# Kernel optimization log

Measured on AMD Instinct MI355X. Metric: run time of the kernel, lower is better.

Reference implementation:

```python
import jax, jax.numpy as jnp
import numpy as np

NEG = -1e30

def setup_inputs() -> dict:
    key = jax.random.key(0)
    k1, k2, k3, k4, k5 = jax.random.split(key, 5)
    B, N, M, D = 32, 2048, 512, 512
    C = jax.random.normal(k1, (B, N, D), dtype=jnp.float32)
    Q = jax.random.normal(k2, (B, M, D), dtype=jnp.float32)
    Cmask = jax.random.randint(k3, (B, N), 0, 2, dtype=jnp.int32)
    Qmask = jax.random.randint(k4, (B, M), 0, 2, dtype=jnp.int32)
    # Linear(3*dim, 1, bias=False) weight, flattened to a (3*dim,) vector.
    bound = 1.0 / np.sqrt(3 * D)
    w = jax.random.uniform(k5, (3 * D,), dtype=jnp.float32, minval=-bound, maxval=bound)
    return {"C": C, "Q": Q, "Cmask": Cmask, "Qmask": Qmask, "w": w}

def reference(C, Q, Cmask, Qmask, w):
    D = C.shape[-1]
    w1, w2, w3 = w[:D], w[D:2 * D], w[2 * D:]
    # Trilinear similarity, decomposed: S = w1.Ct + w2.Qt + w3.(Ct*Qt)
    S = (jnp.einsum('bnd,d->bn', C, w1)[:, :, None]
         + jnp.einsum('bmd,d->bm', Q, w2)[:, None, :]
         + jnp.einsum('bnd,bmd->bnm', C * w3, Q))  # [B, N, M]
    Qm = Qmask.astype(S.dtype)[:, None, :]  # [B, 1, M]; 1 = masked
    Cm = Cmask.astype(S.dtype)[:, :, None]  # [B, N, 1]
    S1 = jax.nn.softmax(S * (1.0 - Qm) + Qm * NEG, axis=2)
    S2 = jax.nn.softmax(S * (1.0 - Cm) + Cm * NEG, axis=1)
    A = jnp.einsum('bnm,bmd->bnd', S1, Q)
    T = jnp.einsum('bnm,bnd->bmd', S2, C)     # S2^T @ C
    Bout = jnp.einsum('bnm,bmd->bnd', S1, T)  # S1 @ (S2^T @ C)
    return (A, Bout)
```

## Files before the change

### kernel.cpp

```cpp
#include <hip/hip_runtime.h>

#define BB 32
#define NN 2048
#define MM 512
#define DD 512

typedef _Float16 half8f __attribute__((ext_vector_type(8)));
typedef float    f32x16 __attribute__((ext_vector_type(16)));

#define MFMA __builtin_amdgcn_mfma_f32_32x32x16_f16

__device__ __forceinline__ int pidx(int r, int k, int K) {
    return (r >> 7) * (K << 7) + ((k >> 4) << 11) + (((r >> 5) & 3) << 9)
         + (((r & 31) + (((k >> 3) & 1) << 5)) << 3) + (k & 7);
}
__device__ __forceinline__ int kpart(int k) {
    return ((k >> 4) << 11) + (((k >> 3) & 1) << 8) + (k & 7);
}

__device__ __forceinline__ void glds16(const void* g, void* l) {
    __builtin_amdgcn_global_load_lds(
        (const __attribute__((address_space(1))) unsigned int*)g,
        (__attribute__((address_space(3))) unsigned int*)l, 16, 0, 0);
}

__global__ __launch_bounds__(256) void k_prepC(const float* __restrict__ C, const float* __restrict__ w,
                                               float* __restrict__ c1, _Float16* __restrict__ PCt,
                                               _Float16* __restrict__ PCh, _Float16* __restrict__ PCl) {
    __shared__ float Ls[64][65];
    const int bid = blockIdx.x;
    const int b   = bid >> 8;
    const int nn0 = ((bid >> 3) & 31) << 6;
    const int dd0 = (bid & 7) << 6;
    const int tid = threadIdx.x;
    const int nl  = tid >> 2;
    const int dl  = (tid & 3) << 4;
    const float* w1 = w;
    const float* w3 = w + 2 * DD;
    const size_t crow = ((size_t)(b * NN + nn0 + nl)) * DD + dd0 + dl;
    float4 v[4], u[4], t[4];
#pragma unroll
    for (int p = 0; p < 4; ++p) {
        v[p] = *(const float4*)(C + crow + p * 4);
        u[p] = *(const float4*)(w1 + dd0 + dl + p * 4);
        t[p] = *(const float4*)(w3 + dd0 + dl + p * 4);
    }
    float s = 0.f;
#pragma unroll
    for (int p = 0; p < 4; ++p) s += v[p].x * u[p].x + v[p].y * u[p].y + v[p].z * u[p].z + v[p].w * u[p].w;
    s += __shfl_xor(s, 1); s += __shfl_xor(s, 2);
    if ((tid & 3) == 0) atomicAdd(&c1[b * NN + nn0 + nl], s);
#pragma unroll
    for (int p = 0; p < 4; ++p) {
        Ls[dl + p * 4 + 0][nl] = v[p].x; Ls[dl + p * 4 + 1][nl] = v[p].y;
        Ls[dl + p * 4 + 2][nl] = v[p].z; Ls[dl + p * 4 + 3][nl] = v[p].w;
    }
    const size_t pb = (size_t)b * NN * DD;
#pragma unroll
    for (int q = 0; q < 2; ++q) {
        float x[8];
#pragma unroll
        for (int e = 0; e < 8; ++e) {
            const int p = q * 2 + (e >> 2);
            const float* vp = &v[p].x; const float* tp = &t[p].x;
            x[e] = vp[e & 3] * tp[e & 3];
        }
        half8f hh, ll;
#pragma unroll
        for (int e = 0; e < 8; ++e) {
            _Float16 h = (_Float16)x[e]; hh[e] = h;
            ll[e] = (_Float16)((x[e] - (float)h) * 2048.f);
        }
        const int pi = pidx(nn0 + nl, dd0 + dl + q * 8, DD);
        *(half8f*)&PCh[pb + pi] = hh;
        *(half8f*)&PCl[pb + pi] = ll;
    }
    __syncthreads();
    const int d2 = tid >> 2, n2 = (tid & 3) << 4;
    const size_t tb = (size_t)b * DD * NN;
#pragma unroll
    for (int q = 0; q < 2; ++q) {
        const int nc = n2 + q * 8;
        half8f o;
#pragma unroll
        for (int j = 0; j < 8; ++j) o[j] = (_Float16)Ls[d2][nc + j];
        *(half8f*)&PCt[tb + pidx(dd0 + d2, nn0 + nc, NN)] = o;
    }
}

__global__ __launch_bounds__(256) void k_prepQ(const float* __restrict__ Q, const int* __restrict__ Qmask,
                                               const float* __restrict__ w, float* __restrict__ q2,
                                               _Float16* __restrict__ PQt,
                                               _Float16* __restrict__ PQh, _Float16* __restrict__ PQl) {
    __shared__ float Ls[64][65];
    const int bid = blockIdx.x;
    const int b   = bid >> 6;
    const int rem = bid & 63;
    const int mm0 = (rem >> 3) << 6;
    const int dd0 = (rem & 7) << 6;
    const int tid = threadIdx.x;
    const int ml  = tid >> 2;
    const int dl  = (tid & 3) << 4;
    const float* w2 = w + DD;
    const size_t qrow = ((size_t)(b * MM + mm0 + ml)) * DD + dd0 + dl;
    float4 v[4], u[4];
#pragma unroll
    for (int p = 0; p < 4; ++p) {
        v[p] = *(const float4*)(Q + qrow + p * 4);
        u[p] = *(const float4*)(w2 + dd0 + dl + p * 4);
    }
    float s = 0.f;
#pragma unroll
    for (int p = 0; p < 4; ++p) s += v[p].x * u[p].x + v[p].y * u[p].y + v[p].z * u[p].z + v[p].w * u[p].w;
    s += __shfl_xor(s, 1); s += __shfl_xor(s, 2);
    if ((tid & 3) == 0) atomicAdd(&q2[b * MM + mm0 + ml], s);
    const float z = Qmask[b * MM + mm0 + ml] ? 0.f : 1.f;
#pragma unroll
    for (int p = 0; p < 4; ++p) {
        Ls[dl + p * 4 + 0][ml] = v[p].x * z; Ls[dl + p * 4 + 1][ml] = v[p].y * z;
        Ls[dl + p * 4 + 2][ml] = v[p].z * z; Ls[dl + p * 4 + 3][ml] = v[p].w * z;
    }
    const size_t pb = (size_t)b * MM * DD;
#pragma unroll
    for (int q = 0; q < 2; ++q) {
        float x[8];
#pragma unroll
        for (int e = 0; e < 8; ++e) {
            const int p = q * 2 + (e >> 2);
            const float* vp = &v[p].x;
            x[e] = vp[e & 3];
        }
        half8f hh, ll;
#pragma unroll
        for (int e = 0; e < 8; ++e) {
            _Float16 h = (_Float16)x[e]; hh[e] = h;
            ll[e] = (_Float16)((x[e] - (float)h) * 2048.f);
        }
        const int pi = pidx(mm0 + ml, dd0 + dl + q * 8, DD);
        *(half8f*)&PQh[pb + pi] = hh;
        *(half8f*)&PQl[pb + pi] = ll;
    }
    __syncthreads();
    const int d2 = tid >> 2, m2 = (tid & 3) << 4;
    const size_t tb = (size_t)b * DD * MM;
#pragma unroll
    for (int q = 0; q < 2; ++q) {
        const int mc = m2 + q * 8;
        half8f o;
#pragma unroll
        for (int j = 0; j < 8; ++j) o[j] = (_Float16)Ls[d2][mc + j];
        *(half8f*)&PQt[tb + pidx(dd0 + d2, mm0 + mc, MM)] = o;
    }
}

__global__ __launch_bounds__(256) void k_te(const _Float16* __restrict__ PE, const int* __restrict__ Cmask,
                                            _Float16* __restrict__ PEt) {
    __shared__ float Ls[64][65];
    const int bid = blockIdx.x;
    const int b   = bid >> 8;
    const int nn0 = ((bid >> 3) & 31) << 6;
    const int mm0 = (bid & 7) << 6;
    const int tid = threadIdx.x;
    const int nl  = tid >> 2;
    const int ml  = (tid & 3) << 4;
    const float z = Cmask[b * NN + nn0 + nl] ? 0.f : 1.f;
    const size_t eb = (size_t)b * NN * MM;
#pragma unroll
    for (int q = 0; q < 2; ++q) {
        half8f v = *(const half8f*)&PE[eb + pidx(nn0 + nl, mm0 + ml + q * 8, MM)];
#pragma unroll
        for (int j = 0; j < 8; ++j) Ls[ml + q * 8 + j][nl] = (float)v[j] * z;
    }
    __syncthreads();
    const int m2 = tid >> 2, n2 = (tid & 3) << 4;
    const size_t tb = (size_t)b * MM * NN;
#pragma unroll
    for (int q = 0; q < 2; ++q) {
        const int nc = n2 + q * 8;
        half8f o;
#pragma unroll
        for (int j = 0; j < 8; ++j) o[j] = (_Float16)Ls[m2][nc + j];
        *(half8f*)&PEt[tb + pidx(mm0 + m2, nn0 + nc, NN)] = o;
    }
}

__global__ __launch_bounds__(256, 2) void k_sgemm(const _Float16* __restrict__ PCh, const _Float16* __restrict__ PCl,
                                                  const _Float16* __restrict__ PQh, const _Float16* __restrict__ PQl,
                                                  const int* __restrict__ Cmask, const int* __restrict__ Qmask,
                                                  const float* __restrict__ c1, const float* __restrict__ q2,
                                                  _Float16* __restrict__ E, float* __restrict__ rsum,
                                                  float* __restrict__ csum) {
    __shared__ _Float16 SB[2][16384];
    __shared__ float rowp[128], colp[128], cmz[128], qmz[128], c1s[128], q2s[128];
    const int hw  = blockIdx.x;
    const int bid = ((hw & 7) << 8) | (hw >> 3);
    const int b   = bid >> 6;
    const int rem = bid & 63;
    const int n0  = (rem >> 2) << 7;
    const int m0  = (rem & 3) << 7;
    const int tid = threadIdx.x;
    const int lane = tid & 63;
    const int wv   = tid >> 6;
    const int wr = wv >> 1, wc = wv & 1;
    if (tid < 128) {
        rowp[tid] = 0.f; colp[tid] = 0.f;
        cmz[tid] = Cmask[b * NN + n0 + tid] ? 0.f : 1.f;
        c1s[tid] = c1[b * NN + n0 + tid];
    } else {
        const int t = tid - 128;
        qmz[t] = Qmask[b * MM + m0 + t] ? 0.f : 1.f;
        q2s[t] = q2[b * MM + m0 + t];
    }
    const half8f* gAh = (const half8f*)(PCh + (size_t)b * NN * DD + (size_t)n0 * DD) + lane;
    const half8f* gAl = (const half8f*)(PCl + (size_t)b * NN * DD + (size_t)n0 * DD) + lane;
    const half8f* gBh = (const half8f*)(PQh + (size_t)b * MM * DD + (size_t)m0 * DD) + lane;
    const half8f* gBl = (const half8f*)(PQl + (size_t)b * MM * DD + (size_t)m0 * DD) + lane;
    const half8f* srcj[8]; int offj[8];
#pragma unroll
    for (int j = 0; j < 8; ++j) {
        const int f = j * 4 + wv;
        const int kcl = f >> 4, t = f & 15;
        const half8f* s; int p;
        if (t < 4)       { s = gAh; p = t; }
        else if (t < 8)  { s = gAl; p = t - 4; }
        else if (t < 12) { s = gBh; p = t - 8; }
        else             { s = gBl; p = t - 12; }
        srcj[j] = s + kcl * 256 + p * 64;
        offj[j] = (kcl * 16 + t) << 9;
    }
    f32x16 accH[2][2] = {};
    f32x16 accX[2][2] = {};
#pragma unroll
    for (int j = 0; j < 8; ++j) glds16(srcj[j], &SB[0][offj[j]]);
    int cur = 0;
    for (int ks = 0; ks < 16; ++ks) {
        __syncthreads();
        if (ks + 1 < 16) {
#pragma unroll
            for (int j = 0; j < 8; ++j) glds16(srcj[j] + (ks + 1) * 512, &SB[cur ^ 1][offj[j]]);
        }
#pragma unroll
        for (int kcl = 0; kcl < 2; ++kcl) {
            const _Float16* F = &SB[cur][(kcl << 13) + lane * 8];
            half8f ah0 = *(const half8f*)(F + ((2 * wr) << 9));
            half8f ah1 = *(const half8f*)(F + ((2 * wr + 1) << 9));
            half8f al0 = *(const half8f*)(F + ((4 + 2 * wr) << 9));
            half8f al1 = *(const half8f*)(F + ((5 + 2 * wr) << 9));
            half8f bh0 = *(const half8f*)(F + ((8 + 2 * wc) << 9));
            half8f bh1 = *(const half8f*)(F + ((9 + 2 * wc) << 9));
            half8f bl0 = *(const half8f*)(F + ((12 + 2 * wc) << 9));
            half8f bl1 = *(const half8f*)(F + ((13 + 2 * wc) << 9));
            accH[0][0] = MFMA(ah0, bh0, accH[0][0], 0, 0, 0);
            accH[0][1] = MFMA(ah0, bh1, accH[0][1], 0, 0, 0);
            accH[1][0] = MFMA(ah1, bh0, accH[1][0], 0, 0, 0);
            accH[1][1] = MFMA(ah1, bh1, accH[1][1], 0, 0, 0);
            accX[0][0] = MFMA(ah0, bl0, accX[0][0], 0, 0, 0);
            accX[0][0] = MFMA(al0, bh0, accX[0][0], 0, 0, 0);
            accX[0][1] = MFMA(ah0, bl1, accX[0][1], 0, 0, 0);
            accX[0][1] = MFMA(al0, bh1, accX[0][1], 0, 0, 0);
            accX[1][0] = MFMA(ah1, bl0, accX[1][0], 0, 0, 0);
            accX[1][0] = MFMA(al1, bh0, accX[1][0], 0, 0, 0);
            accX[1][1] = MFMA(ah1, bl1, accX[1][1], 0, 0, 0);
            accX[1][1] = MFMA(al1, bh1, accX[1][1], 0, 0, 0);
        }
        cur ^= 1;
    }
    const float inv2k = 4.8828125e-4f;
    const int mcol0 = wc * 64 + (lane & 31);
    const float qz0 = qmz[mcol0], qz1 = qmz[mcol0 + 32];
    const float q2v0 = q2s[mcol0], q2v1 = q2s[mcol0 + 32];
    const int hi4 = (lane >> 5) << 2;
    const size_t ebase = (size_t)b * NN * MM + (size_t)n0 * MM;
    const int kp0 = kpart(m0 + mcol0);
    const int kp1 = kpart(m0 + mcol0 + 32);
    float colacc0 = 0.f, colacc1 = 0.f;
#pragma unroll
    for (int i = 0; i < 2; ++i) {
#pragma unroll
        for (int r = 0; r < 16; ++r) {
            const int nloc = wr * 64 + i * 32 + (r & 3) + ((r >> 2) << 3) + hi4;
            const float base = c1s[nloc];
            float S0 = accH[i][0][r] + accX[i][0][r] * inv2k + base + q2v0;
            float S1 = accH[i][1][r] + accX[i][1][r] * inv2k + base + q2v1;
            float e0 = __expf(S0), e1 = __expf(S1);
            _Float16 h0 = (_Float16)e0, h1 = (_Float16)e1;
            float eq0 = (float)h0, eq1 = (float)h1;
            const int rp = (((nloc >> 5) & 3) << 9) + ((nloc & 31) << 3);
            E[ebase + rp + kp0] = h0;
            E[ebase + rp + kp1] = h1;
            const float cz = cmz[nloc];
            colacc0 += eq0 * cz;
            colacc1 += eq1 * cz;
            float rv = eq0 * qz0 + eq1 * qz1;
            rv += __shfl_xor(rv, 1);  rv += __shfl_xor(rv, 2);
            rv += __shfl_xor(rv, 4);  rv += __shfl_xor(rv, 8);
            rv += __shfl_xor(rv, 16);
            if ((lane & 31) == 0) atomicAdd(&rowp[nloc], rv);
        }
    }
    atomicAdd(&colp[mcol0], colacc0);
    atomicAdd(&colp[mcol0 + 32], colacc1);
    __syncthreads();
    if (tid < 128) atomicAdd(&rsum[b * NN + n0 + tid], rowp[tid]);
    else atomicAdd(&csum[b * MM + m0 + tid - 128], colp[tid - 128]);
}

__global__ __launch_bounds__(256, 2) void k_T(const _Float16* __restrict__ PCt,
                                              const _Float16* __restrict__ PEt,
                                              const float* __restrict__ csum,
                                              const int* __restrict__ Qmask,
                                              _Float16* __restrict__ Tt) {
    __shared__ _Float16 SB[2][16384];
    const int hw  = blockIdx.x;
    const int bid = ((hw & 7) << 6) | (hw >> 3);
    const int b   = bid >> 4;
    const int rem = bid & 15;
    const int d0  = (rem >> 2) << 7;
    const int m0  = (rem & 3) << 7;
    const int tid = threadIdx.x;
    const int lane = tid & 63;
    const int wv   = tid >> 6;
    const int wr = wv >> 1, wc = wv & 1;
    const half8f* gA = (const half8f*)(PCt + (size_t)b * DD * NN + (size_t)d0 * NN) + lane;
    const half8f* gB = (const half8f*)(PEt + (size_t)b * MM * NN + (size_t)m0 * NN) + lane;
    const half8f* srcj[8]; int offj[8];
#pragma unroll
    for (int j = 0; j < 8; ++j) {
        const int f = j * 4 + wv;
        const int kcl = f >> 3, t = f & 7;
        const half8f* s; int p;
        if (t < 4) { s = gA; p = t; } else { s = gB; p = t - 4; }
        srcj[j] = s + kcl * 256 + p * 64;
        offj[j] = (kcl * 8 + t) << 9;
    }
    f32x16 acc[2][2] = {};
#pragma unroll
    for (int j = 0; j < 8; ++j) glds16(srcj[j], &SB[0][offj[j]]);
    int cur = 0;
    for (int ks = 0; ks < 32; ++ks) {
        __syncthreads();
        if (ks + 1 < 32) {
#pragma unroll
            for (int j = 0; j < 8; ++j) glds16(srcj[j] + (ks + 1) * 1024, &SB[cur ^ 1][offj[j]]);
        }
#pragma unroll
        for (int kcl = 0; kcl < 4; ++kcl) {
            const _Float16* F = &SB[cur][(kcl << 12) + lane * 8];
            half8f a0 = *(const half8f*)(F + ((2 * wr) << 9));
            half8f a1 = *(const half8f*)(F + ((2 * wr + 1) << 9));
            half8f b0 = *(const half8f*)(F + ((4 + 2 * wc) << 9));
            half8f b1 = *(const half8f*)(F + ((5 + 2 * wc) << 9));
            acc[0][0] = MFMA(a0, b0, acc[0][0], 0, 0, 0);
            acc[0][1] = MFMA(a0, b1, acc[0][1], 0, 0, 0);
            acc[1][0] = MFMA(a1, b0, acc[1][0], 0, 0, 0);
            acc[1][1] = MFMA(a1, b1, acc[1][1], 0, 0, 0);
        }
        cur ^= 1;
    }
    const int mc0 = m0 + wc * 64 + (lane & 31);
    const float s0 = (Qmask[b * MM + mc0]      ? 0.f : 1.f) / csum[b * MM + mc0];
    const float s1 = (Qmask[b * MM + mc0 + 32] ? 0.f : 1.f) / csum[b * MM + mc0 + 32];
    const int hi4 = (lane >> 5) << 2;
    const size_t tbase = (size_t)b * DD * MM + (size_t)d0 * MM;
    const int kp0 = kpart(mc0);
    const int kp1 = kpart(mc0 + 32);
#pragma unroll
    for (int i = 0; i < 2; ++i) {
#pragma unroll
        for (int r = 0; r < 16; ++r) {
            const int dloc = wr * 64 + i * 32 + (r & 3) + ((r >> 2) << 3) + hi4;
            const int rp = (((dloc >> 5) & 3) << 9) + ((dloc & 31) << 3);
            Tt[tbase + rp + kp0] = (_Float16)(acc[i][0][r] * s0);
            Tt[tbase + rp + kp1] = (_Float16)(acc[i][1][r] * s1);
        }
    }
}

__global__ __launch_bounds__(256, 2) void k_AB(const _Float16* __restrict__ E,
                                               const _Float16* __restrict__ PQt,
                                               const _Float16* __restrict__ Tt,
                                               const float* __restrict__ rsum,
                                               float* __restrict__ outA, float* __restrict__ outB) {
    __shared__ _Float16 SB[2][12288];
    const int hw  = blockIdx.x;
    const int bid = ((hw & 7) << 8) | (hw >> 3);
    const int b   = bid >> 6;
    const int rem = bid & 63;
    const int n0  = (rem >> 2) << 7;
    const int d0  = (rem & 3) << 7;
    const int tid = threadIdx.x;
    const int lane = tid & 63;
    const int wv   = tid >> 6;
    const int wr = wv >> 1, wc = wv & 1;
    const half8f* gE = (const half8f*)(E   + (size_t)b * NN * MM + (size_t)n0 * MM) + lane;
    const half8f* gQ = (const half8f*)(PQt + (size_t)b * DD * MM + (size_t)d0 * MM) + lane;
    const half8f* gT = (const half8f*)(Tt  + (size_t)b * DD * MM + (size_t)d0 * MM) + lane;
    const half8f* srcj[6]; int offj[6];
#pragma unroll
    for (int j = 0; j < 6; ++j) {
        const int f = j * 4 + wv;
        const int kcl = (f >= 12) ? 1 : 0;
        const int t = f - kcl * 12;
        const half8f* s; int p;
        if (t < 4)      { s = gE; p = t; }
        else if (t < 8) { s = gQ; p = t - 4; }
        else            { s = gT; p = t - 8; }
        srcj[j] = s + kcl * 256 + p * 64;
        offj[j] = (kcl * 12 + t) << 9;
    }
    f32x16 accA[2][2] = {};
    f32x16 accB[2][2] = {};
#pragma unroll
    for (int j = 0; j < 6; ++j) glds16(srcj[j], &SB[0][offj[j]]);
    int cur = 0;
    for (int ks = 0; ks < 16; ++ks) {
        __syncthreads();
        if (ks + 1 < 16) {
#pragma unroll
            for (int j = 0; j < 6; ++j) glds16(srcj[j] + (ks + 1) * 512, &SB[cur ^ 1][offj[j]]);
        }
#pragma unroll
        for (int kcl = 0; kcl < 2; ++kcl) {
            const _Float16* F = &SB[cur][kcl * 6144 + lane * 8];
            half8f e0 = *(const half8f*)(F + ((2 * wr) << 9));
            half8f e1 = *(const half8f*)(F + ((2 * wr + 1) << 9));
            half8f q0 = *(const half8f*)(F + ((4 + 2 * wc) << 9));
            half8f q1 = *(const half8f*)(F + ((5 + 2 * wc) << 9));
            half8f t0 = *(const half8f*)(F + ((8 + 2 * wc) << 9));
            half8f t1 = *(const half8f*)(F + ((9 + 2 * wc) << 9));
            accA[0][0] = MFMA(e0, q0, accA[0][0], 0, 0, 0);
            accA[0][1] = MFMA(e0, q1, accA[0][1], 0, 0, 0);
            accA[1][0] = MFMA(e1, q0, accA[1][0], 0, 0, 0);
            accA[1][1] = MFMA(e1, q1, accA[1][1], 0, 0, 0);
            accB[0][0] = MFMA(e0, t0, accB[0][0], 0, 0, 0);
            accB[0][1] = MFMA(e0, t1, accB[0][1], 0, 0, 0);
            accB[1][0] = MFMA(e1, t0, accB[1][0], 0, 0, 0);
            accB[1][1] = MFMA(e1, t1, accB[1][1], 0, 0, 0);
        }
        cur ^= 1;
    }
    const int dc = d0 + wc * 64 + (lane & 31);
#pragma unroll
    for (int i = 0; i < 2; ++i) {
#pragma unroll
        for (int r = 0; r < 16; ++r) {
            const int row = (r & 3) + ((r >> 2) << 3) + ((lane >> 5) << 2);
            const int n = n0 + wr * 64 + i * 32 + row;
            const float inv = __builtin_amdgcn_rcpf(rsum[b * NN + n]);
            const size_t o = ((size_t)(b * NN + n)) * DD + dc;
            outA[o]      = accA[i][0][r] * inv;
            outA[o + 32] = accA[i][1][r] * inv;
            outB[o]      = accB[i][0][r] * inv;
            outB[o + 32] = accB[i][1][r] * inv;
        }
    }
}

extern "C" void kernel_launch(void* const* d_in, const int* in_sizes, int n_in,
                              void* d_out, int out_size, void* d_ws, size_t ws_size,
                              hipStream_t stream) {
    const float* C = (const float*)d_in[0];
    const float* Q = (const float*)d_in[1];
    const int* Cmask = (const int*)d_in[2];
    const int* Qmask = (const int*)d_in[3];
    const float* w  = (const float*)d_in[4];

    const size_t BNM = (size_t)BB * NN * MM;
    const size_t BMD = (size_t)BB * MM * DD;
    const size_t BND = (size_t)BB * NN * DD;
    const size_t BN  = (size_t)BB * NN;
    const size_t BM  = (size_t)BB * MM;

    _Float16* E   = (_Float16*)d_ws;
    _Float16* Tt  = E + BNM;
    _Float16* PQt = Tt + BMD;
    float* c1   = (float*)(PQt + BMD);
    float* q2   = c1 + BN;
    float* rsum = q2 + BM;
    float* csum = rsum + BN;

    _Float16* PCt = (_Float16*)d_out;
    _Float16* PCh = PCt + BND;
    _Float16* PCl = PCh + BND;
    _Float16* PQh = PCl + BND;
    _Float16* PQl = PQh + BMD;
    _Float16* PEt = PCh;

    hipMemsetAsync(c1, 0, 2 * (BN + BM) * sizeof(float), stream);

    k_prepQ<<<BB * 64, 256, 0, stream>>>(Q, Qmask, w, q2, PQt, PQh, PQl);
    k_prepC<<<BB * 256, 256, 0, stream>>>(C, w, c1, PCt, PCh, PCl);
    k_sgemm<<<2048, 256, 0, stream>>>(PCh, PCl, PQh, PQl, Cmask, Qmask, c1, q2, E, rsum, csum);
    k_te<<<BB * 256, 256, 0, stream>>>(E, Cmask, PEt);
    k_T<<<512, 256, 0, stream>>>(PCt, PEt, csum, Qmask, Tt);
    k_AB<<<2048, 256, 0, stream>>>(E, PQt, Tt, rsum,
                                   (float*)d_out, (float*)d_out + BND);
}
```

Before: 727.5 us.

## Drop hi/lo fp16 split in S GEMM and fuse E transpose into epilogue

The similarity GEMM no longer uses a split-fp16 (high plus scaled low residual) representation, so it computes one fp16 MFMA product instead of three and stops writing and reading the low-part buffers. The separate transpose kernel for E is removed; the GEMM epilogue now writes the Cmask-scaled transposed E directly with scattered scalar stores. The smaller LDS footprint allows launch bounds of three blocks per SM. The risk is lower accuracy in the logits before exp, plus uncoalesced 2-byte stores in the epilogue.

```diff
diff --git a/kernel.cpp b/kernel.cpp
--- a/kernel.cpp
+++ b/kernel.cpp
@@ -26,7 +26,7 @@
 
 __global__ __launch_bounds__(256) void k_prepC(const float* __restrict__ C, const float* __restrict__ w,
                                                float* __restrict__ c1, _Float16* __restrict__ PCt,
-                                               _Float16* __restrict__ PCh, _Float16* __restrict__ PCl) {
+                                               _Float16* __restrict__ PCh) {
     __shared__ float Ls[64][65];
     const int bid = blockIdx.x;
     const int b   = bid >> 8;
@@ -58,22 +58,14 @@
     const size_t pb = (size_t)b * NN * DD;
 #pragma unroll
     for (int q = 0; q < 2; ++q) {
-        float x[8];
+        half8f hh;
 #pragma unroll
         for (int e = 0; e < 8; ++e) {
             const int p = q * 2 + (e >> 2);
             const float* vp = &v[p].x; const float* tp = &t[p].x;
-            x[e] = vp[e & 3] * tp[e & 3];
-        }
-        half8f hh, ll;
-#pragma unroll
-        for (int e = 0; e < 8; ++e) {
-            _Float16 h = (_Float16)x[e]; hh[e] = h;
-            ll[e] = (_Float16)((x[e] - (float)h) * 2048.f);
-        }
-        const int pi = pidx(nn0 + nl, dd0 + dl + q * 8, DD);
-        *(half8f*)&PCh[pb + pi] = hh;
-        *(half8f*)&PCl[pb + pi] = ll;
+            hh[e] = (_Float16)(vp[e & 3] * tp[e & 3]);
+        }
+        *(half8f*)&PCh[pb + pidx(nn0 + nl, dd0 + dl + q * 8, DD)] = hh;
     }
     __syncthreads();
     const int d2 = tid >> 2, n2 = (tid & 3) << 4;
@@ -90,8 +82,7 @@
 
 __global__ __launch_bounds__(256) void k_prepQ(const float* __restrict__ Q, const int* __restrict__ Qmask,
                                                const float* __restrict__ w, float* __restrict__ q2,
-                                               _Float16* __restrict__ PQt,
-                                               _Float16* __restrict__ PQh, _Float16* __restrict__ PQl) {
+                                               _Float16* __restrict__ PQt, _Float16* __restrict__ PQh) {
     __shared__ float Ls[64][65];
     const int bid = blockIdx.x;
     const int b   = bid >> 6;
@@ -123,22 +114,14 @@
     const size_t pb = (size_t)b * MM * DD;
 #pragma unroll
     for (int q = 0; q < 2; ++q) {
-        float x[8];
+        half8f hh;
 #pragma unroll
         for (int e = 0; e < 8; ++e) {
             const int p = q * 2 + (e >> 2);
             const float* vp = &v[p].x;
-            x[e] = vp[e & 3];
-        }
-        half8f hh, ll;
-#pragma unroll
-        for (int e = 0; e < 8; ++e) {
-            _Float16 h = (_Float16)x[e]; hh[e] = h;
-            ll[e] = (_Float16)((x[e] - (float)h) * 2048.f);
-        }
-        const int pi = pidx(mm0 + ml, dd0 + dl + q * 8, DD);
-        *(half8f*)&PQh[pb + pi] = hh;
-        *(half8f*)&PQl[pb + pi] = ll;
+            hh[e] = (_Float16)vp[e & 3];
+        }
+        *(half8f*)&PQh[pb + pidx(mm0 + ml, dd0 + dl + q * 8, DD)] = hh;
     }
     __syncthreads();
     const int d2 = tid >> 2, m2 = (tid & 3) << 4;
@@ -153,44 +136,13 @@
     }
 }
 
-__global__ __launch_bounds__(256) void k_te(const _Float16* __restrict__ PE, const int* __restrict__ Cmask,
-                                            _Float16* __restrict__ PEt) {
-    __shared__ float Ls[64][65];
-    const int bid = blockIdx.x;
-    const int b   = bid >> 8;
-    const int nn0 = ((bid >> 3) & 31) << 6;
-    const int mm0 = (bid & 7) << 6;
-    const int tid = threadIdx.x;
-    const int nl  = tid >> 2;
-    const int ml  = (tid & 3) << 4;
-    const float z = Cmask[b * NN + nn0 + nl] ? 0.f : 1.f;
-    const size_t eb = (size_t)b * NN * MM;
-#pragma unroll
-    for (int q = 0; q < 2; ++q) {
-        half8f v = *(const half8f*)&PE[eb + pidx(nn0 + nl, mm0 + ml + q * 8, MM)];
-#pragma unroll
-        for (int j = 0; j < 8; ++j) Ls[ml + q * 8 + j][nl] = (float)v[j] * z;
-    }
-    __syncthreads();
-    const int m2 = tid >> 2, n2 = (tid & 3) << 4;
-    const size_t tb = (size_t)b * MM * NN;
-#pragma unroll
-    for (int q = 0; q < 2; ++q) {
-        const int nc = n2 + q * 8;
-        half8f o;
-#pragma unroll
-        for (int j = 0; j < 8; ++j) o[j] = (_Float16)Ls[m2][nc + j];
-        *(half8f*)&PEt[tb + pidx(mm0 + m2, nn0 + nc, NN)] = o;
-    }
-}
-
-__global__ __launch_bounds__(256, 2) void k_sgemm(const _Float16* __restrict__ PCh, const _Float16* __restrict__ PCl,
-                                                  const _Float16* __restrict__ PQh, const _Float16* __restrict__ PQl,
+__global__ __launch_bounds__(256, 3) void k_sgemm(const _Float16* __restrict__ PCh,
+                                                  const _Float16* __restrict__ PQh,
                                                   const int* __restrict__ Cmask, const int* __restrict__ Qmask,
                                                   const float* __restrict__ c1, const float* __restrict__ q2,
-                                                  _Float16* __restrict__ E, float* __restrict__ rsum,
-                                                  float* __restrict__ csum) {
-    __shared__ _Float16 SB[2][16384];
+                                                  _Float16* __restrict__ E, _Float16* __restrict__ PEt,
+                                                  float* __restrict__ rsum, float* __restrict__ csum) {
+    __shared__ _Float16 SB[2][8192];
     __shared__ float rowp[128], colp[128], cmz[128], qmz[128], c1s[128], q2s[128];
     const int hw  = blockIdx.x;
     const int bid = ((hw & 7) << 8) | (hw >> 3);
@@ -211,61 +163,40 @@
         qmz[t] = Qmask[b * MM + m0 + t] ? 0.f : 1.f;
         q2s[t] = q2[b * MM + m0 + t];
     }
-    const half8f* gAh = (const half8f*)(PCh + (size_t)b * NN * DD + (size_t)n0 * DD) + lane;
-    const half8f* gAl = (const half8f*)(PCl + (size_t)b * NN * DD + (size_t)n0 * DD) + lane;
-    const half8f* gBh = (const half8f*)(PQh + (size_t)b * MM * DD + (size_t)m0 * DD) + lane;
-    const half8f* gBl = (const half8f*)(PQl + (size_t)b * MM * DD + (size_t)m0 * DD) + lane;
-    const half8f* srcj[8]; int offj[8];
-#pragma unroll
-    for (int j = 0; j < 8; ++j) {
+    const half8f* gA = (const half8f*)(PCh + (size_t)b * NN * DD + (size_t)n0 * DD) + lane;
+    const half8f* gB = (const half8f*)(PQh + (size_t)b * MM * DD + (size_t)m0 * DD) + lane;
+    const half8f* srcj[4]; int offj[4];
+#pragma unroll
+    for (int j = 0; j < 4; ++j) {
         const int f = j * 4 + wv;
-        const int kcl = f >> 4, t = f & 15;
-        const half8f* s; int p;
-        if (t < 4)       { s = gAh; p = t; }
-        else if (t < 8)  { s = gAl; p = t - 4; }
-        else if (t < 12) { s = gBh; p = t - 8; }
-        else             { s = gBl; p = t - 12; }
-        srcj[j] = s + kcl * 256 + p * 64;
-        offj[j] = (kcl * 16 + t) << 9;
-    }
-    f32x16 accH[2][2] = {};
-    f32x16 accX[2][2] = {};
-#pragma unroll
-    for (int j = 0; j < 8; ++j) glds16(srcj[j], &SB[0][offj[j]]);
+        const int kcl = f >> 3, t = f & 7;
+        srcj[j] = (t < 4 ? gA + t * 64 : gB + (t - 4) * 64) + kcl * 256;
+        offj[j] = (kcl * 8 + t) << 9;
+    }
+    f32x16 acc[2][2] = {};
+#pragma unroll
+    for (int j = 0; j < 4; ++j) glds16(srcj[j], &SB[0][offj[j]]);
     int cur = 0;
     for (int ks = 0; ks < 16; ++ks) {
         __syncthreads();
         if (ks + 1 < 16) {
 #pragma unroll
-            for (int j = 0; j < 8; ++j) glds16(srcj[j] + (ks + 1) * 512, &SB[cur ^ 1][offj[j]]);
+            for (int j = 0; j < 4; ++j) glds16(srcj[j] + (ks + 1) * 512, &SB[cur ^ 1][offj[j]]);
         }
 #pragma unroll
         for (int kcl = 0; kcl < 2; ++kcl) {
-            const _Float16* F = &SB[cur][(kcl << 13) + lane * 8];
-            half8f ah0 = *(const half8f*)(F + ((2 * wr) << 9));
-            half8f ah1 = *(const half8f*)(F + ((2 * wr + 1) << 9));
-            half8f al0 = *(const half8f*)(F + ((4 + 2 * wr) << 9));
-            half8f al1 = *(const half8f*)(F + ((5 + 2 * wr) << 9));
-            half8f bh0 = *(const half8f*)(F + ((8 + 2 * wc) << 9));
-            half8f bh1 = *(const half8f*)(F + ((9 + 2 * wc) << 9));
-            half8f bl0 = *(const half8f*)(F + ((12 + 2 * wc) << 9));
-            half8f bl1 = *(const half8f*)(F + ((13 + 2 * wc) << 9));
-            accH[0][0] = MFMA(ah0, bh0, accH[0][0], 0, 0, 0);
-            accH[0][1] = MFMA(ah0, bh1, accH[0][1], 0, 0, 0);
-            accH[1][0] = MFMA(ah1, bh0, accH[1][0], 0, 0, 0);
-            accH[1][1] = MFMA(ah1, bh1, accH[1][1], 0, 0, 0);
-            accX[0][0] = MFMA(ah0, bl0, accX[0][0], 0, 0, 0);
-            accX[0][0] = MFMA(al0, bh0, accX[0][0], 0, 0, 0);
-            accX[0][1] = MFMA(ah0, bl1, accX[0][1], 0, 0, 0);
-            accX[0][1] = MFMA(al0, bh1, accX[0][1], 0, 0, 0);
-            accX[1][0] = MFMA(ah1, bl0, accX[1][0], 0, 0, 0);
-            accX[1][0] = MFMA(al1, bh0, accX[1][0], 0, 0, 0);
-            accX[1][1] = MFMA(ah1, bl1, accX[1][1], 0, 0, 0);
-            accX[1][1] = MFMA(al1, bh1, accX[1][1], 0, 0, 0);
+            const _Float16* F = &SB[cur][(kcl << 12) + lane * 8];
+            half8f a0 = *(const half8f*)(F + ((2 * wr) << 9));
+            half8f a1 = *(const half8f*)(F + ((2 * wr + 1) << 9));
+            half8f b0 = *(const half8f*)(F + ((4 + 2 * wc) << 9));
+            half8f b1 = *(const half8f*)(F + ((5 + 2 * wc) << 9));
+            acc[0][0] = MFMA(a0, b0, acc[0][0], 0, 0, 0);
+            acc[0][1] = MFMA(a0, b1, acc[0][1], 0, 0, 0);
+            acc[1][0] = MFMA(a1, b0, acc[1][0], 0, 0, 0);
+            acc[1][1] = MFMA(a1, b1, acc[1][1], 0, 0, 0);
         }
         cur ^= 1;
     }
-    const float inv2k = 4.8828125e-4f;
     const int mcol0 = wc * 64 + (lane & 31);
     const float qz0 = qmz[mcol0], qz1 = qmz[mcol0 + 32];
     const float q2v0 = q2s[mcol0], q2v1 = q2s[mcol0 + 32];
@@ -273,6 +204,9 @@
     const size_t ebase = (size_t)b * NN * MM + (size_t)n0 * MM;
     const int kp0 = kpart(m0 + mcol0);
     const int kp1 = kpart(m0 + mcol0 + 32);
+    const size_t petb = (size_t)b * MM * NN;
+    const int mp0 = ((m0 + mcol0) >> 7) * (NN << 7) + (((mcol0 >> 5) & 3) << 9) + ((lane & 31) << 3);
+    const int mp1 = ((m0 + mcol0 + 32) >> 7) * (NN << 7) + ((((mcol0 + 32) >> 5) & 3) << 9) + ((lane & 31) << 3);
     float colacc0 = 0.f, colacc1 = 0.f;
 #pragma unroll
     for (int i = 0; i < 2; ++i) {
@@ -280,8 +214,8 @@
         for (int r = 0; r < 16; ++r) {
             const int nloc = wr * 64 + i * 32 + (r & 3) + ((r >> 2) << 3) + hi4;
             const float base = c1s[nloc];
-            float S0 = accH[i][0][r] + accX[i][0][r] * inv2k + base + q2v0;
-            float S1 = accH[i][1][r] + accX[i][1][r] * inv2k + base + q2v1;
+            float S0 = acc[i][0][r] + base + q2v0;
+            float S1 = acc[i][1][r] + base + q2v1;
             float e0 = __expf(S0), e1 = __expf(S1);
             _Float16 h0 = (_Float16)e0, h1 = (_Float16)e1;
             float eq0 = (float)h0, eq1 = (float)h1;
@@ -289,6 +223,9 @@
             E[ebase + rp + kp0] = h0;
             E[ebase + rp + kp1] = h1;
             const float cz = cmz[nloc];
+            const int kpn = kpart(n0 + nloc);
+            PEt[petb + mp0 + kpn] = (_Float16)(eq0 * cz);
+            PEt[petb + mp1 + kpn] = (_Float16)(eq1 * cz);
             colacc0 += eq0 * cz;
             colacc1 += eq1 * cz;
             float rv = eq0 * qz0 + eq1 * qz1;
@@ -481,17 +418,14 @@
 
     _Float16* PCt = (_Float16*)d_out;
     _Float16* PCh = PCt + BND;
-    _Float16* PCl = PCh + BND;
-    _Float16* PQh = PCl + BND;
-    _Float16* PQl = PQh + BMD;
-    _Float16* PEt = PCh;
+    _Float16* PQh = PCh + BND;
+    _Float16* PEt = PQh + BMD;
 
     hipMemsetAsync(c1, 0, 2 * (BN + BM) * sizeof(float), stream);
 
-    k_prepQ<<<BB * 64, 256, 0, stream>>>(Q, Qmask, w, q2, PQt, PQh, PQl);
-    k_prepC<<<BB * 256, 256, 0, stream>>>(C, w, c1, PCt, PCh, PCl);
-    k_sgemm<<<2048, 256, 0, stream>>>(PCh, PCl, PQh, PQl, Cmask, Qmask, c1, q2, E, rsum, csum);
-    k_te<<<BB * 256, 256, 0, stream>>>(E, Cmask, PEt);
+    k_prepQ<<<BB * 64, 256, 0, stream>>>(Q, Qmask, w, q2, PQt, PQh);
+    k_prepC<<<BB * 256, 256, 0, stream>>>(C, w, c1, PCt, PCh);
+    k_sgemm<<<2048, 256, 0, stream>>>(PCh, PQh, Cmask, Qmask, c1, q2, E, PEt, rsum, csum);
     k_T<<<512, 256, 0, stream>>>(PCt, PEt, csum, Qmask, Tt);
     k_AB<<<2048, 256, 0, stream>>>(E, PQt, Tt, rsum,
                                    (float*)d_out, (float*)d_out + BND);
```

Result: faster. 655.8 us (-9.9%).
